# Performance work log

Hardware: AMD Instinct MI355X
Metric: run time of the kernel (lower is better)

Reference implementation:

```python
import jax, jax.numpy as jnp
import numpy as np

E, S, D, A, L, H, C = 8, 6000, 128, 16, 64, 256, 64
B = 50            # no_batches hardcoded in torch forward
T = S // B        # number of outer integration steps
DT = 0.5          # solver dt; t_horizon=[0,1] -> 2 reversible-Heun substeps
NSUB = 2
SQDT = float(np.sqrt(DT))


def setup_inputs():
    ks = jax.random.split(jax.random.key(0), 24)
    w = lambda k, shp, s=0.05: (jax.random.normal(k, shp) * s).astype(jnp.float32)
    z = lambda shp: jnp.zeros(shp, jnp.float32)
    return dict(
        xs=w(ks[0], (E, S, D), 1.0),
        actions=w(ks[1], (E, S, A), 1.0),
        z0_noise=w(ks[2], (T, E, B, L), 1.0),
        dW=w(ks[3], (T, NSUB, E * B, L), 1.0),
        enc_w1=w(ks[4], (E, D, H)), enc_b1=z((E, H)),
        enc_w2=w(ks[5], (E, H, C)), enc_b2=z((E, C)),
        qz0_w=w(ks[6], (E, C, 2 * L)), qz0_b=z((E, 2 * L)),
        act_w=w(ks[7], (E, L + A + D, L)), act_b=z((E, L)),
        fw1=w(ks[8], (L, H)), fb1=z((H,)),
        fw2=w(ks[9], (H, H)), fb2=z((H,)),
        fw3=w(ks[10], (H, L)), fb3=z((L,)),
        hw1=w(ks[11], (L, H)), hb1=z((H,)),
        hw2=w(ks[12], (H, H)), hb2=z((H,)),
        hw3=w(ks[13], (H, L)), hb3=z((L,)),
        gw1=w(ks[14], (L, H)), gb1=z((L, H)),
        gw2=w(ks[15], (L, H), 0.02), gb2=jnp.ones((L,), jnp.float32),
        pw1=w(ks[16], (E, L, H)), pb1=z((E, H)),
        pw2=w(ks[17], (E, H, H)), pb2=z((E, H)),
        pw3=w(ks[18], (E, H, D)), pb3=z((E, D)),
        pz0_mean=z((E, 1, L)), pz0_logstd=z((E, 1, L)),
    )


def reference(xs, actions, z0_noise, dW,
              enc_w1, enc_b1, enc_w2, enc_b2, qz0_w, qz0_b, act_w, act_b,
              fw1, fb1, fw2, fb2, fw3, fb3, hw1, hb1, hw2, hb2, hw3, hb3,
              gw1, gb1, gw2, gb2, pw1, pb1, pw2, pb2, pw3, pb3,
              pz0_mean, pz0_logstd):
    xs_r = xs.reshape(E, T, B, D).transpose(1, 0, 2, 3)       # [T,E,B,D]
    act_r = actions.reshape(E, T, B, A).transpose(1, 0, 2, 3)  # [T,E,B,A]

    def mlp3(y, w1, b1, w2, b2, w3, b3):
        h1 = jax.nn.sigmoid(y @ w1 + b1)
        h2 = jax.nn.sigmoid(h1 @ w2 + b2)
        return h2 @ w3 + b3

    def g_fn(y):  # per-latent-dim diagonal diffusion nets, vectorized over L
        hc = jax.nn.sigmoid(y[..., None] * gw1 + gb1)          # [N,L,H]
        return jnp.sum(hc * gw2, axis=-1) + gb2                # [N,L]

    def drift_all(zc):
        fz = mlp3(zc, fw1, fb1, fw2, fb2, fw3, fb3)
        hz = mlp3(zc, hw1, hb1, hw2, hb2, hw3, hb3)
        gz = g_fn(zc)
        u = (fz - hz) / gz
        return fz, gz, 0.5 * jnp.sum(u * u, axis=-1)           # logqp drift

    def sde_solve(zini, dWs):  # reversible Heun, Stratonovich, logqp-augmented
        zc = zh = zini
        lc = lh = jnp.zeros(zini.shape[0], zini.dtype)
        fz, gz, lf = drift_all(zc)
        for k in range(NSUB):
            dWk = dWs[k] * SQDT
            zh_n = 2.0 * zc - zh + fz * DT + gz * dWk
            lh_n = 2.0 * lc - lh + lf * DT
            fz1, gz1, lf1 = drift_all(zh_n)
            zc = zc + 0.5 * (fz + fz1) * DT + 0.5 * (gz + gz1) * dWk
            lc = lc + 0.5 * (lf + lf1) * DT
            zh, lh, fz, gz, lf = zh_n, lh_n, fz1, gz1, lf1
        return zc, lc

    def step(z_prev, inp):
        i, x_i, a_i, n_i, dW_i = inp
        c1 = jax.nn.sigmoid(jnp.einsum('ebd,edh->ebh', x_i, enc_w1) + enc_b1[:, None])
        ctx = jnp.einsum('ebh,ehc->ebc', c1, enc_w2) + enc_b2[:, None]
        q = jnp.einsum('ebc,eck->ebk', ctx, qz0_w) + qz0_b[:, None]
        qm, ql = q[..., :L], q[..., L:]
        z0 = qm + jnp.exp(ql) * n_i
        z_in = jnp.where(i == 0, z0, z_prev)
        lat = jnp.concatenate([z_in, a_i, x_i], axis=-1)
        z_enc = jnp.einsum('ebf,efl->ebl', lat, act_w) + act_b[:, None]
        zf, lr = sde_solve(z_enc.reshape(E * B, L), dW_i)
        z_new = zf.reshape(E, B, L)
        p1 = jax.nn.sigmoid(jnp.einsum('ebl,elh->ebh', z_new, pw1) + pb1[:, None])
        p2 = jax.nn.sigmoid(jnp.einsum('ebh,ehk->ebk', p1, pw2) + pb2[:, None])
        xm = jnp.einsum('ebh,ehd->ebd', p2, pw3) + pb3[:, None]
        # KL(q(z0) || p(z0)) elementwise, p has mean pz0_mean, logstd pz0_logstd
        kl = (pz0_logstd - ql
              + (jnp.exp(2.0 * ql) + (qm - pz0_mean) ** 2) / (2.0 * jnp.exp(2.0 * pz0_logstd))
              - 0.5)
        logqp0 = kl.sum(-1).mean(-1)  # [E]
        return z_new, (xm, lr.reshape(E, B), logqp0)

    z_init = jnp.zeros((E, B, L), xs.dtype)
    _, (xm_all, lr_all, lq0_all) = jax.lax.scan(
        step, z_init, (jnp.arange(T), xs_r, act_r, z0_noise, dW))
    predicted_xs = xm_all.transpose(1, 0, 2, 3).reshape(E, T * B, D)
    logqp_path = lr_all.mean(-1).sum(0) + lq0_all.sum(0)  # [E]
    return logqp_path, predicted_xs
```

## Files before the change

### kernel.cpp

```cpp
#include <hip/hip_runtime.h>
#include <math.h>

#define E 8
#define S 6000
#define D 128
#define A 16
#define L 64
#define H 256
#define C 64
#define B 50
#define T 120
#define NSUB 2
#define FLAT 208
#define RTOT 400
#define RPB 10
#define NBLK (RTOT / RPB)
#define BGRP 10
#define NBG 5

#define DT 0.5f
#define SQDT 0.70710678118654752440f

#define GNT 4096
#define GYMIN (-128.0f)
#define GDY 0.0625f
#define GINVDY 16.0f

typedef __attribute__((ext_vector_type(8))) short bf16x8;
typedef __attribute__((ext_vector_type(4))) float f32x4;

#define MFMA16(a, b, c) __builtin_amdgcn_mfma_f32_16x16x32_bf16(a, b, c, 0, 0, 0)

__device__ __forceinline__ float sigf(float x) { return 1.0f / (1.0f + __expf(-x)); }

__device__ __forceinline__ unsigned short f2bf(float x) {
    union { float f; unsigned u; } v; v.f = x;
    unsigned r = (v.u + 0x7FFFu + ((v.u >> 16) & 1u)) >> 16;
    return (unsigned short)r;
}

__global__ void gtab_kernel(const float* __restrict__ gw1, const float* __restrict__ gb1,
                            const float* __restrict__ gw2, const float* __restrict__ gb2,
                            float* __restrict__ tab) {
    int idx = blockIdx.x * blockDim.x + threadIdx.x;
    if (idx >= L * GNT) return;
    int l = idx / GNT, i = idx % GNT;
    float y = GYMIN + (float)i * GDY;
    const float* w1 = gw1 + l * H;
    const float* b1 = gb1 + l * H;
    const float* w2 = gw2 + l * H;
    float acc = gb2[l];
    #pragma unroll 4
    for (int h = 0; h < H; ++h) acc += w2[h] * sigf(y * w1[h] + b1[h]);
    tab[idx] = acc;
}

__global__ void packB_kernel(const float* __restrict__ src, unsigned short* __restrict__ dst,
                             int K, int N) {
    int idx = blockIdx.x * 256 + threadIdx.x;
    if (idx >= K * N) return;
    int j = idx & 7;
    int lane = (idx >> 3) & 63;
    int t2 = idx >> 9;
    int KC = K >> 5;
    int kc = t2 % KC, n = t2 / KC;
    int k = (kc << 5) + ((lane >> 4) << 3) + j;
    int c = (n << 4) + (lane & 15);
    dst[idx] = f2bf(src[k * N + c]);
}

__global__ void packAW_kernel(const float* __restrict__ aw, unsigned short* __restrict__ dst) {
    int idx = blockIdx.x * 256 + threadIdx.x;
    if (idx >= E * L * L) return;
    int e = idx >> 12;
    int rem = idx & 4095;
    int j = rem & 7;
    int lane = (rem >> 3) & 63;
    int t2 = rem >> 9;
    int kc = t2 & 1, n = t2 >> 1;
    int k = (kc << 5) + ((lane >> 4) << 3) + j;
    int c = (n << 4) + (lane & 15);
    dst[idx] = f2bf(aw[((size_t)e * FLAT + k) * L + c]);
}

__global__ __launch_bounds__(256) void enc_kernel(const float* __restrict__ xs, const float* __restrict__ z0n,
                           const float* __restrict__ ew1, const float* __restrict__ eb1,
                           const float* __restrict__ ew2, const float* __restrict__ eb2,
                           const float* __restrict__ qw,  const float* __restrict__ qb,
                           const float* __restrict__ pm,  const float* __restrict__ pl,
                           float* __restrict__ z0buf, float* __restrict__ logqp0p) {
    int bid = blockIdx.x;
    int bg = bid % NBG; int te = bid / NBG; int e = te % E; int t = te / E;
    int tid = threadIdx.x;
    __shared__ float xsh[BGRP][D];
    __shared__ float c1s[BGRP][H];
    __shared__ float part[4][C][BGRP];
    __shared__ float ctxs[BGRP][C];
    __shared__ float qs[BGRP][2 * L];

    for (int i = tid; i < BGRP * D; i += 256) {
        int j = i / D, d = i % D;
        xsh[j][d] = xs[((size_t)e * S + (size_t)t * B + bg * BGRP + j) * D + d];
    }
    __syncthreads();
    {
        float bias = eb1[e * H + tid];
        float acc[BGRP];
        #pragma unroll
        for (int j = 0; j < BGRP; ++j) acc[j] = bias;
        const float* w = ew1 + (size_t)e * D * H + tid;
        #pragma unroll 4
        for (int d = 0; d < D; ++d) {
            float wv = w[(size_t)d * H];
            #pragma unroll
            for (int j = 0; j < BGRP; ++j) acc[j] += xsh[j][d] * wv;
        }
        #pragma unroll
        for (int j = 0; j < BGRP; ++j) c1s[j][tid] = sigf(acc[j]);
    }
    __syncthreads();
    {
        int c = tid & 63, kq = tid >> 6;
        float acc[BGRP];
        #pragma unroll
        for (int j = 0; j < BGRP; ++j) acc[j] = 0.f;
        const float* w = ew2 + (size_t)e * H * C + c;
        #pragma unroll 4
        for (int h = kq * 64; h < kq * 64 + 64; ++h) {
            float wv = w[(size_t)h * C];
            #pragma unroll
            for (int j = 0; j < BGRP; ++j) acc[j] += c1s[j][h] * wv;
        }
        #pragma unroll
        for (int j = 0; j < BGRP; ++j) part[kq][c][j] = acc[j];
    }
    __syncthreads();
    if (tid < C) {
        float bias = eb2[e * C + tid];
        #pragma unroll
        for (int j = 0; j < BGRP; ++j)
            ctxs[j][tid] = part[0][tid][j] + part[1][tid][j] + part[2][tid][j] + part[3][tid][j] + bias;
    }
    __syncthreads();
    if (tid < 2 * L) {
        float bias = qb[e * 2 * L + tid];
        float acc[BGRP];
        #pragma unroll
        for (int j = 0; j < BGRP; ++j) acc[j] = bias;
        const float* w = qw + (size_t)e * C * 2 * L + tid;
        #pragma unroll 4
        for (int c = 0; c < C; ++c) {
            float wv = w[(size_t)c * 2 * L];
            #pragma unroll
            for (int j = 0; j < BGRP; ++j) acc[j] += ctxs[j][c] * wv;
        }
        #pragma unroll
        for (int j = 0; j < BGRP; ++j) qs[j][tid] = acc[j];
    }
    __syncthreads();
    if (tid < L) {
        int l = tid;
        float kacc = 0.f;
        float m = pm[e * L + l], ls = pl[e * L + l];
        float inv2e = 1.0f / (2.0f * __expf(2.0f * ls));
        #pragma unroll
        for (int j = 0; j < BGRP; ++j) {
            float qm = qs[j][l], ql = qs[j][L + l];
            if (t == 0) {
                int b = bg * BGRP + j;
                float n = z0n[((size_t)e * B + b) * L + l];
                z0buf[((size_t)e * B + b) * L + l] = qm + __expf(ql) * n;
            }
            float dq = qm - m;
            kacc += ls - ql + (__expf(2.f * ql) + dq * dq) * inv2e - 0.5f;
        }
        #pragma unroll
        for (int off = 32; off; off >>= 1) kacc += __shfl_xor(kacc, off);
        if (l == 0) logqp0p[bid] = kacc / (float)B;
    }
}

__global__ __launch_bounds__(64) void ax_kernel(const float* __restrict__ xs, const float* __restrict__ actions,
                          const float* __restrict__ aw, const float* __restrict__ ab,
                          float* __restrict__ ax) {
    int bid = blockIdx.x;
    int bg = bid % NBG; int te = bid / NBG; int e = te % E; int t = te / E;
    int tid = threadIdx.x;
    __shared__ float xrow[BGRP][D];
    __shared__ float arow[BGRP][A];
    for (int i = tid; i < BGRP * D; i += 64) {
        int j = i / D, d = i % D;
        xrow[j][d] = xs[((size_t)e * S + (size_t)t * B + bg * BGRP + j) * D + d];
    }
    for (int i = tid; i < BGRP * A; i += 64) {
        int j = i / A, a = i % A;
        arow[j][a] = actions[((size_t)e * S + (size_t)t * B + bg * BGRP + j) * A + a];
    }
    __syncthreads();
    int l = tid;
    float acc[BGRP];
    float bias = ab[e * L + l];
    #pragma unroll
    for (int j = 0; j < BGRP; ++j) acc[j] = bias;
    const float* awp = aw + ((size_t)e * FLAT + L) * L + l;
    #pragma unroll 4
    for (int a = 0; a < A; ++a) {
        float wv = awp[(size_t)a * L];
        #pragma unroll
        for (int j = 0; j < BGRP; ++j) acc[j] += arow[j][a] * wv;
    }
    const float* xwp = aw + ((size_t)e * FLAT + L + A) * L + l;
    #pragma unroll 4
    for (int d = 0; d < D; ++d) {
        float wv = xwp[(size_t)d * L];
        #pragma unroll
        for (int j = 0; j < BGRP; ++j) acc[j] += xrow[j][d] * wv;
    }
    size_t rbase = (size_t)t * RTOT + e * B + bg * BGRP;
    #pragma unroll
    for (int j = 0; j < BGRP; ++j) ax[(rbase + j) * L + l] = acc[j];
}

__global__ __launch_bounds__(1024, 4) void seq_kernel(
    const unsigned short* __restrict__ pkAW, const float* __restrict__ dW,
    const float* __restrict__ z0buf, const float* __restrict__ axbuf,
    const unsigned short* __restrict__ pk1, const unsigned short* __restrict__ pk2,
    const unsigned short* __restrict__ pk3,
    const float* __restrict__ fb1, const float* __restrict__ hb1,
    const float* __restrict__ fb2, const float* __restrict__ hb2,
    const float* __restrict__ fb3, const float* __restrict__ hb3,
    const float* __restrict__ gtab, float* __restrict__ z_all, float* __restrict__ rowlr)
{
    __shared__ __align__(16) bf16x8 w1L[64 * 64];
    __shared__ __align__(16) bf16x8 w0L[8 * 64];
    __shared__ __align__(16) unsigned short ybf[16 * 64];
    __shared__ __align__(16) unsigned short o1[2][16 * 256];
    __shared__ __align__(16) unsigned short o2[2][16 * 256];
    __shared__ float fh2[2][2][16][64];
    __shared__ float zcS[16][64];

    int tid = threadIdx.x;
    int wv = tid >> 6;
    int lane = tid & 63;
    int rA = lane & 15, kg = lane >> 4;
    int sw = (rA & 7) << 3;
    int r_base = blockIdx.x * RPB;
    int e = blockIdx.x / 5;

    int net = wv >> 3;
    int na = (wv & 7) << 1;
    int cnet = wv >> 3, crem = wv & 7, n0c = crem >> 1, khc = crem & 1;

    {
        const bf16x8* p1 = (const bf16x8*)pk1;
        #pragma unroll
        for (int f = 0; f < 4; ++f)
            w1L[(((wv << 2) + f) << 6) + lane] =
                p1[net * 2048 + ((na + (f >> 1)) * 2 + (f & 1)) * 64 + lane];
        if (wv < 4) {
            const bf16x8* p0 = (const bf16x8*)pkAW + (e << 9);
            w0L[(((wv << 1) + 0) << 6) + lane] = p0[(wv * 2 + 0) * 64 + lane];
            w0L[(((wv << 1) + 1) << 6) + lane] = p0[(wv * 2 + 1) * 64 + lane];
        }
    }
    bf16x8 W2r[16], W3r[4];
    {
        const bf16x8* p2 = (const bf16x8*)pk2 + net * 8192;
        #pragma unroll
        for (int i2 = 0; i2 < 2; ++i2)
            #pragma unroll
            for (int kc = 0; kc < 8; ++kc)
                W2r[i2 * 8 + kc] = p2[((na + i2) * 8 + kc) * 64 + lane];
        const bf16x8* p3 = (const bf16x8*)pk3 + cnet * 2048;
        #pragma unroll
        for (int kc = 0; kc < 4; ++kc)
            W3r[kc] = p3[(n0c * 8 + khc * 4 + kc) * 64 + lane];
    }
    float biasA0, biasA1, biasB0, biasB1, biasC;
    {
        const float* b1 = net ? hb1 : fb1;
        const float* b2 = net ? hb2 : fb2;
        const float* b3 = cnet ? hb3 : fb3;
        biasA0 = b1[((na + 0) << 4) + rA];
        biasA1 = b1[((na + 1) << 4) + rA];
        biasB0 = b2[((na + 0) << 4) + rA];
        biasB1 = b2[((na + 1) << 4) + rA];
        biasC = khc ? 0.f : b3[(n0c << 4) + rA];
    }

    int orow = tid >> 6, ol = tid & 63;
    bool owner = (tid < RPB * L);
    float zc_r = 0.f, zh_r = 0.f, fz_r = 0.f, gz_r = 1.f, lf_r = 0.f;
    float lcacc = 0.f, lrs = 0.f;
    float gt0 = 1.f, gt1 = 1.f, gfr = 0.f;
    float ax_r = 0.f, dwA_r = 0.f, dwB_r = 0.f;

    for (int i = tid; i < 16 * 64; i += 1024) {
        int r = i >> 6;
        float v = (i < RPB * L) ? z0buf[(size_t)r_base * L + i] : 0.f;
        ybf[i ^ ((r & 7) << 3)] = f2bf(v);
    }
    __syncthreads();

    auto gprep = [&](float v) {
        float x = (v - GYMIN) * GINVDY;
        x = fminf(fmaxf(x, 0.0f), (float)(GNT - 2) + 0.999f);
        int ii = (int)x;
        gfr = x - (float)ii;
        const float* tl = gtab + ((size_t)ol << 12);
        gt0 = tl[ii];
        gt1 = tl[ii + 1];
    };

    auto drift3 = [&]() {
        {
            bf16x8 A0 = *(const bf16x8*)&ybf[((rA << 6) + (kg << 3)) ^ sw];
            bf16x8 A1 = *(const bf16x8*)&ybf[((rA << 6) + 32 + (kg << 3)) ^ sw];
            f32x4 acc0 = (f32x4){biasA0, biasA0, biasA0, biasA0};
            f32x4 acc1 = (f32x4){biasA1, biasA1, biasA1, biasA1};
            acc0 = MFMA16(A0, w1L[(((wv << 2) + 0) << 6) + lane], acc0);
            acc0 = MFMA16(A1, w1L[(((wv << 2) + 1) << 6) + lane], acc0);
            acc1 = MFMA16(A0, w1L[(((wv << 2) + 2) << 6) + lane], acc1);
            acc1 = MFMA16(A1, w1L[(((wv << 2) + 3) << 6) + lane], acc1);
            unsigned short* o1n = o1[net];
            int c0 = ((na + 0) << 4) + rA;
            int c1 = ((na + 1) << 4) + rA;
            #pragma unroll
            for (int rr = 0; rr < 4; ++rr) {
                int r = (kg << 2) + rr;
                int rx = (r & 7) << 3;
                o1n[((r << 8) + c0) ^ rx] = f2bf(sigf(acc0[rr]));
                o1n[((r << 8) + c1) ^ rx] = f2bf(sigf(acc1[rr]));
            }
        }
        __syncthreads();
        {
            const unsigned short* o1n = o1[net];
            f32x4 acc0 = (f32x4){biasB0, biasB0, biasB0, biasB0};
            f32x4 acc1 = (f32x4){biasB1, biasB1, biasB1, biasB1};
            #pragma unroll
            for (int kc = 0; kc < 8; ++kc) {
                bf16x8 Ak = *(const bf16x8*)&o1n[((rA << 8) + (kc << 5) + (kg << 3)) ^ sw];
                acc0 = MFMA16(Ak, W2r[kc], acc0);
                acc1 = MFMA16(Ak, W2r[8 + kc], acc1);
            }
            unsigned short* o2n = o2[net];
            int c0 = ((na + 0) << 4) + rA;
            int c1 = ((na + 1) << 4) + rA;
            #pragma unroll
            for (int rr = 0; rr < 4; ++rr) {
                int r = (kg << 2) + rr;
                int rx = (r & 7) << 3;
                o2n[((r << 8) + c0) ^ rx] = f2bf(sigf(acc0[rr]));
                o2n[((r << 8) + c1) ^ rx] = f2bf(sigf(acc1[rr]));
            }
        }
        __syncthreads();
        {
            const unsigned short* o2n = o2[cnet];
            f32x4 acc = (f32x4){biasC, biasC, biasC, biasC};
            #pragma unroll
            for (int kc = 0; kc < 4; ++kc) {
                bf16x8 Ak = *(const bf16x8*)&o2n[((rA << 8) + (((khc << 2) + kc) << 5) + (kg << 3)) ^ sw];
                acc = MFMA16(Ak, W3r[kc], acc);
            }
            int c = (n0c << 4) + rA;
            #pragma unroll
            for (int rr = 0; rr < 4; ++rr)
                fh2[cnet][khc][(kg << 2) + rr][c] = acc[rr];
        }
        __syncthreads();
    };

    for (int t = 0; t < T; ++t) {
        if (owner) {
            ax_r  = axbuf[((size_t)t * RTOT + r_base) * L + tid];
            dwA_r = dW[((size_t)(t * 2 + 0) * RTOT + r_base) * L + tid] * SQDT;
            dwB_r = dW[((size_t)(t * 2 + 1) * RTOT + r_base) * L + tid] * SQDT;
        }
        if (wv < 4) {
            bf16x8 Z0 = *(const bf16x8*)&ybf[((rA << 6) + (kg << 3)) ^ sw];
            bf16x8 Z1 = *(const bf16x8*)&ybf[((rA << 6) + 32 + (kg << 3)) ^ sw];
            f32x4 acc = (f32x4){0.f, 0.f, 0.f, 0.f};
            acc = MFMA16(Z0, w0L[((wv << 1) << 6) + lane], acc);
            acc = MFMA16(Z1, w0L[(((wv << 1) + 1) << 6) + lane], acc);
            int c = (wv << 4) + rA;
            #pragma unroll
            for (int rr = 0; rr < 4; ++rr)
                zcS[(kg << 2) + rr][c] = acc[rr];
        }
        __syncthreads();
        if (owner) {
            float v = zcS[orow][ol] + ax_r;
            zc_r = v;
            ybf[tid ^ ((orow & 7) << 3)] = f2bf(v);
            gprep(v);
        }
        __syncthreads();

        #pragma unroll
        for (int d = 0; d < 3; ++d) {
            drift3();
            if (owner) {
                float fv = fh2[0][0][orow][ol] + fh2[0][1][orow][ol];
                float hv = fh2[1][0][orow][ol] + fh2[1][1][orow][ol];
                float gv = gt0 * (1.0f - gfr) + gt1 * gfr;
                float uu = (fv - hv) / gv;
                float us = uu * uu;
                #pragma unroll
                for (int off = 32; off; off >>= 1) us += __shfl_xor(us, off);
                float lfd = 0.5f * us;
                if (d == 0) {
                    fz_r = fv; gz_r = gv; lf_r = lfd;
                    float y1 = zc_r + fv * DT + gv * dwA_r;
                    zh_r = y1;
                    ybf[tid ^ ((orow & 7) << 3)] = f2bf(y1);
                    gprep(y1);
                } else if (d == 1) {
                    zc_r += 0.5f * (fz_r + fv) * DT + 0.5f * (gz_r + gv) * dwA_r;
                    lcacc = 0.5f * (lf_r + lfd) * DT;
                    float y2 = 2.f * zc_r - zh_r + fv * DT + gv * dwB_r;
                    fz_r = fv; gz_r = gv; lf_r = lfd;
                    ybf[tid ^ ((orow & 7) << 3)] = f2bf(y2);
                    gprep(y2);
                } else {
                    zc_r += 0.5f * (fz_r + fv) * DT + 0.5f * (gz_r + gv) * dwB_r;
                    lcacc += 0.5f * (lf_r + lfd) * DT;
                    lrs += lcacc;
                    z_all[((size_t)t * RTOT + r_base) * L + tid] = zc_r;
                    ybf[tid ^ ((orow & 7) << 3)] = f2bf(zc_r);
                }
            }
            __syncthreads();
        }
    }
    if (owner && ol == 0) rowlr[r_base + orow] = lrs;
}

__global__ __launch_bounds__(256) void proj_kernel(const float* __restrict__ z_all,
                            const float* __restrict__ pw1, const float* __restrict__ pb1,
                            const float* __restrict__ pw2, const float* __restrict__ pb2,
                            const float* __restrict__ pw3, const float* __restrict__ pb3,
                            float* __restrict__ out) {
    int bid = blockIdx.x;
    int bg = bid % NBG; int te = bid / NBG; int e = te % E; int t = te / E;
    int tid = threadIdx.x;
    __shared__ float zs[BGRP][L];
    __shared__ float p1s[BGRP][H];
    __shared__ float p2s[BGRP][H];
    __shared__ float part3[D][BGRP];
    size_t rbase = (size_t)t * RTOT + e * B + bg * BGRP;
    for (int i = tid; i < BGRP * L; i += 256) {
        int j = i >> 6, ll = i & 63;
        zs[j][ll] = z_all[(rbase + j) * L + ll];
    }
    __syncthreads();
    {
        float bias = pb1[e * H + tid];
        float acc[BGRP];
        #pragma unroll
        for (int j = 0; j < BGRP; ++j) acc[j] = bias;
        const float* w = pw1 + (size_t)e * L * H + tid;
        #pragma unroll 4
        for (int k = 0; k < L; ++k) {
            float wv = w[(size_t)k * H];
            #pragma unroll
            for (int j = 0; j < BGRP; ++j) acc[j] += zs[j][k] * wv;
        }
        #pragma unroll
        for (int j = 0; j < BGRP; ++j) p1s[j][tid] = sigf(acc[j]);
    }
    __syncthreads();
    {
        float bias = pb2[e * H + tid];
        float acc[BGRP];
        #pragma unroll
        for (int j = 0; j < BGRP; ++j) acc[j] = bias;
        const float* w = pw2 + (size_t)e * H * H + tid;
        #pragma unroll 4
        for (int k = 0; k < H; ++k) {
            float wv = w[(size_t)k * H];
            #pragma unroll
            for (int j = 0; j < BGRP; ++j) acc[j] += p1s[j][k] * wv;
        }
        #pragma unroll
        for (int j = 0; j < BGRP; ++j) p2s[j][tid] = sigf(acc[j]);
    }
    __syncthreads();
    float acc3[BGRP];
    {
        int dd = tid & 127, kh = tid >> 7;
        #pragma unroll
        for (int j = 0; j < BGRP; ++j) acc3[j] = 0.f;
        const float* w = pw3 + (size_t)e * H * D + dd;
        #pragma unroll 4
        for (int k = kh * 128; k < kh * 128 + 128; ++k) {
            float wv = w[(size_t)k * D];
            #pragma unroll
            for (int j = 0; j < BGRP; ++j) acc3[j] += p2s[j][k] * wv;
        }
        if (kh == 1) {
            #pragma unroll
            for (int j = 0; j < BGRP; ++j) part3[dd][j] = acc3[j];
        }
    }
    __syncthreads();
    if (tid < D) {
        float bias = pb3[e * D + tid];
        #pragma unroll
        for (int j = 0; j < BGRP; ++j) {
            out[8 + ((size_t)e * S + (size_t)t * B + bg * BGRP + j) * D + tid]
                = acc3[j] + part3[tid][j] + bias;
        }
    }
}

__global__ void fin_kernel(const float* __restrict__ logqp0p, const float* __restrict__ rowlr,
                           float* __restrict__ out) {
    int e = threadIdx.x;
    if (e < E) {
        float acc = 0.f;
        for (int t = 0; t < T; ++t)
            for (int bg = 0; bg < NBG; ++bg)
                acc += logqp0p[(t * E + e) * NBG + bg];
        float s = 0.f;
        for (int b = 0; b < B; ++b) s += rowlr[e * B + b];
        out[e] = acc + s / (float)B;
    }
}

extern "C" void kernel_launch(void* const* d_in, const int* in_sizes, int n_in,
                              void* d_out, int out_size, void* d_ws, size_t ws_size,
                              hipStream_t stream) {
    const float* xs      = (const float*)d_in[0];
    const float* actions = (const float*)d_in[1];
    const float* z0n     = (const float*)d_in[2];
    const float* dWp     = (const float*)d_in[3];
    const float* ew1     = (const float*)d_in[4];
    const float* eb1     = (const float*)d_in[5];
    const float* ew2     = (const float*)d_in[6];
    const float* eb2     = (const float*)d_in[7];
    const float* qw      = (const float*)d_in[8];
    const float* qb      = (const float*)d_in[9];
    const float* aw      = (const float*)d_in[10];
    const float* ab      = (const float*)d_in[11];
    const float* fw1     = (const float*)d_in[12];
    const float* fb1     = (const float*)d_in[13];
    const float* fw2     = (const float*)d_in[14];
    const float* fb2     = (const float*)d_in[15];
    const float* fw3     = (const float*)d_in[16];
    const float* fb3     = (const float*)d_in[17];
    const float* hw1     = (const float*)d_in[18];
    const float* hb1     = (const float*)d_in[19];
    const float* hw2     = (const float*)d_in[20];
    const float* hb2     = (const float*)d_in[21];
    const float* hw3     = (const float*)d_in[22];
    const float* hb3     = (const float*)d_in[23];
    const float* gw1     = (const float*)d_in[24];
    const float* gb1     = (const float*)d_in[25];
    const float* gw2     = (const float*)d_in[26];
    const float* gb2     = (const float*)d_in[27];
    const float* pw1     = (const float*)d_in[28];
    const float* pb1     = (const float*)d_in[29];
    const float* pw2     = (const float*)d_in[30];
    const float* pb2     = (const float*)d_in[31];
    const float* pw3     = (const float*)d_in[32];
    const float* pb3     = (const float*)d_in[33];
    const float* pm      = (const float*)d_in[34];
    const float* pl      = (const float*)d_in[35];

    float* ws      = (float*)d_ws;
    float* z0buf   = ws;
    float* axbuf   = z0buf + 25600;
    float* z_all   = axbuf + 3072000;
    float* logqp0p = z_all + 3072000;
    float* rowlr   = logqp0p + 4800;
    float* gtab    = rowlr + 400;
    unsigned short* pku = (unsigned short*)(gtab + 262144);
    unsigned short* pk1 = pku;
    unsigned short* pk2 = pk1 + 32768;
    unsigned short* pk3 = pk2 + 131072;
    unsigned short* pkAW = pk3 + 32768;
    float* out     = (float*)d_out;

    packB_kernel<<<64,  256, 0, stream>>>(fw1, pk1,          64, 256);
    packB_kernel<<<64,  256, 0, stream>>>(hw1, pk1 + 16384,  64, 256);
    packB_kernel<<<256, 256, 0, stream>>>(fw2, pk2,          256, 256);
    packB_kernel<<<256, 256, 0, stream>>>(hw2, pk2 + 65536,  256, 256);
    packB_kernel<<<64,  256, 0, stream>>>(fw3, pk3,          256, 64);
    packB_kernel<<<64,  256, 0, stream>>>(hw3, pk3 + 16384,  256, 64);
    packAW_kernel<<<128, 256, 0, stream>>>(aw, pkAW);
    gtab_kernel<<<1024, 256, 0, stream>>>(gw1, gb1, gw2, gb2, gtab);
    enc_kernel<<<T * E * NBG, 256, 0, stream>>>(xs, z0n, ew1, eb1, ew2, eb2, qw, qb, pm, pl, z0buf, logqp0p);
    ax_kernel<<<T * E * NBG, 64, 0, stream>>>(xs, actions, aw, ab, axbuf);
    seq_kernel<<<NBLK, 1024, 0, stream>>>(pkAW, dWp, z0buf, axbuf,
                                          pk1, pk2, pk3,
                                          fb1, hb1, fb2, hb2, fb3, hb3,
                                          gtab, z_all, rowlr);
    proj_kernel<<<T * E * NBG, 256, 0, stream>>>(z_all, pw1, pb1, pw2, pb2, pw3, pb3, out);
    fin_kernel<<<1, 64, 0, stream>>>(logqp0p, rowlr, out);
}
```

Before: 2.973 ms.

## Trim barriers and defer logqp reduction in the sequential SDE kernel

Restructures the serial SDE loop in several ways. The z-encoder MFMA now writes directly into the drift input with the ax term added in-register, which removes one block barrier per step. A second ybf buffer separates the carried state from the drift input. The per-substep logqp wavefront shuffle-reduction is replaced by a per-lane weighted accumulation that is reduced once at the end. __syncthreads is replaced by a custom barrier that waits only on LDS counters, and the encoder weights are held in registers. The risks are ordering hazards with the lighter barrier and a change in floating-point summation order.

```diff
diff --git a/kernel.cpp b/kernel.cpp
--- a/kernel.cpp
+++ b/kernel.cpp
@@ -39,6 +39,12 @@
     return (unsigned short)r;
 }
 
+__device__ __forceinline__ void bar_lgkm() {
+    asm volatile("s_waitcnt lgkmcnt(0)" ::: "memory");
+    __builtin_amdgcn_s_barrier();
+    __builtin_amdgcn_sched_barrier(0);
+}
+
 __global__ void gtab_kernel(const float* __restrict__ gw1, const float* __restrict__ gb1,
                             const float* __restrict__ gw2, const float* __restrict__ gb2,
                             float* __restrict__ tab) {
@@ -231,11 +237,11 @@
     const float* __restrict__ fb3, const float* __restrict__ hb3,
     const float* __restrict__ gtab, float* __restrict__ z_all, float* __restrict__ rowlr)
 {
-    __shared__ __align__(16) bf16x8 w1L[64 * 64];
-    __shared__ __align__(16) bf16x8 w0L[8 * 64];
-    __shared__ __align__(16) unsigned short ybf[16 * 64];
-    __shared__ __align__(16) unsigned short o1[2][16 * 256];
-    __shared__ __align__(16) unsigned short o2[2][16 * 256];
+    __shared__ __align__(16) bf16x8 w1L[4096];
+    __shared__ __align__(16) unsigned short ybfA[1024];
+    __shared__ __align__(16) unsigned short ybfZ[1024];
+    __shared__ __align__(16) unsigned short o1[2][4096];
+    __shared__ __align__(16) unsigned short o2[2][4096];
     __shared__ float fh2[2][2][16][64];
     __shared__ float zcS[16][64];
 
@@ -247,23 +253,20 @@
     int r_base = blockIdx.x * RPB;
     int e = blockIdx.x / 5;
 
+    for (int i = tid; i < 4096; i += 1024) w1L[i] = ((const bf16x8*)pk1)[i];
+
     int net = wv >> 3;
     int na = (wv & 7) << 1;
     int cnet = wv >> 3, crem = wv & 7, n0c = crem >> 1, khc = crem & 1;
-
-    {
-        const bf16x8* p1 = (const bf16x8*)pk1;
-        #pragma unroll
-        for (int f = 0; f < 4; ++f)
-            w1L[(((wv << 2) + f) << 6) + lane] =
-                p1[net * 2048 + ((na + (f >> 1)) * 2 + (f & 1)) * 64 + lane];
-        if (wv < 4) {
-            const bf16x8* p0 = (const bf16x8*)pkAW + (e << 9);
-            w0L[(((wv << 1) + 0) << 6) + lane] = p0[(wv * 2 + 0) * 64 + lane];
-            w0L[(((wv << 1) + 1) << 6) + lane] = p0[(wv * 2 + 1) * 64 + lane];
-        }
-    }
-    bf16x8 W2r[16], W3r[4];
+    int nZ = wv & 3;
+    int lZ = (nZ << 4) + rA;
+
+    bf16x8 W0r0 = {}, W0r1 = {}, W2r[16], W3r[4];
+    if (wv < 4) {
+        const bf16x8* p0 = (const bf16x8*)pkAW + (e << 9);
+        W0r0 = p0[(nZ * 2 + 0) * 64 + lane];
+        W0r1 = p0[(nZ * 2 + 1) * 64 + lane];
+    }
     {
         const bf16x8* p2 = (const bf16x8*)pk2 + net * 8192;
         #pragma unroll
@@ -290,15 +293,15 @@
 
     int orow = tid >> 6, ol = tid & 63;
     bool owner = (tid < RPB * L);
-    float zc_r = 0.f, zh_r = 0.f, fz_r = 0.f, gz_r = 1.f, lf_r = 0.f;
-    float lcacc = 0.f, lrs = 0.f;
+    float zc_r = 0.f, zh_r = 0.f, fz_r = 0.f, gz_r = 1.f;
+    float dwA_r = 0.f, dwB_r = 0.f;
     float gt0 = 1.f, gt1 = 1.f, gfr = 0.f;
-    float ax_r = 0.f, dwA_r = 0.f, dwB_r = 0.f;
-
-    for (int i = tid; i < 16 * 64; i += 1024) {
-        int r = i >> 6;
-        float v = (i < RPB * L) ? z0buf[(size_t)r_base * L + i] : 0.f;
-        ybf[i ^ ((r & 7) << 3)] = f2bf(v);
+    float scal = 0.f;
+
+    {
+        int r = tid >> 6;
+        float v = (tid < RPB * L) ? z0buf[(size_t)r_base * L + tid] : 0.f;
+        ybfZ[tid ^ ((r & 7) << 3)] = f2bf(v);
     }
     __syncthreads();
 
@@ -312,129 +315,131 @@
         gt1 = tl[ii + 1];
     };
 
-    auto drift3 = [&]() {
-        {
-            bf16x8 A0 = *(const bf16x8*)&ybf[((rA << 6) + (kg << 3)) ^ sw];
-            bf16x8 A1 = *(const bf16x8*)&ybf[((rA << 6) + 32 + (kg << 3)) ^ sw];
-            f32x4 acc0 = (f32x4){biasA0, biasA0, biasA0, biasA0};
-            f32x4 acc1 = (f32x4){biasA1, biasA1, biasA1, biasA1};
-            acc0 = MFMA16(A0, w1L[(((wv << 2) + 0) << 6) + lane], acc0);
-            acc0 = MFMA16(A1, w1L[(((wv << 2) + 1) << 6) + lane], acc0);
-            acc1 = MFMA16(A0, w1L[(((wv << 2) + 2) << 6) + lane], acc1);
-            acc1 = MFMA16(A1, w1L[(((wv << 2) + 3) << 6) + lane], acc1);
-            unsigned short* o1n = o1[net];
-            int c0 = ((na + 0) << 4) + rA;
-            int c1 = ((na + 1) << 4) + rA;
+    for (int t = 0; t < T; ++t) {
+        if (wv < 4) {
+            float axv[4];
             #pragma unroll
             for (int rr = 0; rr < 4; ++rr) {
                 int r = (kg << 2) + rr;
-                int rx = (r & 7) << 3;
-                o1n[((r << 8) + c0) ^ rx] = f2bf(sigf(acc0[rr]));
-                o1n[((r << 8) + c1) ^ rx] = f2bf(sigf(acc1[rr]));
-            }
-        }
-        __syncthreads();
-        {
-            const unsigned short* o1n = o1[net];
-            f32x4 acc0 = (f32x4){biasB0, biasB0, biasB0, biasB0};
-            f32x4 acc1 = (f32x4){biasB1, biasB1, biasB1, biasB1};
-            #pragma unroll
-            for (int kc = 0; kc < 8; ++kc) {
-                bf16x8 Ak = *(const bf16x8*)&o1n[((rA << 8) + (kc << 5) + (kg << 3)) ^ sw];
-                acc0 = MFMA16(Ak, W2r[kc], acc0);
-                acc1 = MFMA16(Ak, W2r[8 + kc], acc1);
-            }
-            unsigned short* o2n = o2[net];
-            int c0 = ((na + 0) << 4) + rA;
-            int c1 = ((na + 1) << 4) + rA;
+                axv[rr] = (r < RPB) ? axbuf[((size_t)t * RTOT + r_base + r) * L + lZ] : 0.f;
+            }
+            bf16x8 Z0 = *(const bf16x8*)&ybfZ[((rA << 6) + (kg << 3)) ^ sw];
+            bf16x8 Z1 = *(const bf16x8*)&ybfZ[((rA << 6) + 32 + (kg << 3)) ^ sw];
+            f32x4 acc = (f32x4){0.f, 0.f, 0.f, 0.f};
+            acc = MFMA16(Z0, W0r0, acc);
+            acc = MFMA16(Z1, W0r1, acc);
             #pragma unroll
             for (int rr = 0; rr < 4; ++rr) {
                 int r = (kg << 2) + rr;
-                int rx = (r & 7) << 3;
-                o2n[((r << 8) + c0) ^ rx] = f2bf(sigf(acc0[rr]));
-                o2n[((r << 8) + c1) ^ rx] = f2bf(sigf(acc1[rr]));
-            }
-        }
-        __syncthreads();
-        {
-            const unsigned short* o2n = o2[cnet];
-            f32x4 acc = (f32x4){biasC, biasC, biasC, biasC};
-            #pragma unroll
-            for (int kc = 0; kc < 4; ++kc) {
-                bf16x8 Ak = *(const bf16x8*)&o2n[((rA << 8) + (((khc << 2) + kc) << 5) + (kg << 3)) ^ sw];
-                acc = MFMA16(Ak, W3r[kc], acc);
-            }
-            int c = (n0c << 4) + rA;
-            #pragma unroll
-            for (int rr = 0; rr < 4; ++rr)
-                fh2[cnet][khc][(kg << 2) + rr][c] = acc[rr];
-        }
-        __syncthreads();
-    };
-
-    for (int t = 0; t < T; ++t) {
-        if (owner) {
-            ax_r  = axbuf[((size_t)t * RTOT + r_base) * L + tid];
-            dwA_r = dW[((size_t)(t * 2 + 0) * RTOT + r_base) * L + tid] * SQDT;
-            dwB_r = dW[((size_t)(t * 2 + 1) * RTOT + r_base) * L + tid] * SQDT;
-        }
-        if (wv < 4) {
-            bf16x8 Z0 = *(const bf16x8*)&ybf[((rA << 6) + (kg << 3)) ^ sw];
-            bf16x8 Z1 = *(const bf16x8*)&ybf[((rA << 6) + 32 + (kg << 3)) ^ sw];
-            f32x4 acc = (f32x4){0.f, 0.f, 0.f, 0.f};
-            acc = MFMA16(Z0, w0L[((wv << 1) << 6) + lane], acc);
-            acc = MFMA16(Z1, w0L[(((wv << 1) + 1) << 6) + lane], acc);
-            int c = (wv << 4) + rA;
-            #pragma unroll
-            for (int rr = 0; rr < 4; ++rr)
-                zcS[(kg << 2) + rr][c] = acc[rr];
-        }
-        __syncthreads();
-        if (owner) {
-            float v = zcS[orow][ol] + ax_r;
-            zc_r = v;
-            ybf[tid ^ ((orow & 7) << 3)] = f2bf(v);
-            gprep(v);
-        }
-        __syncthreads();
+                float v = acc[rr] + axv[rr];
+                zcS[r][lZ] = v;
+                ybfA[((r << 6) + lZ) ^ ((r & 7) << 3)] = f2bf(v);
+            }
+        }
+        bar_lgkm();
 
         #pragma unroll
         for (int d = 0; d < 3; ++d) {
-            drift3();
+            if (d == 0 && owner) {
+                zc_r = zcS[orow][ol];
+                zh_r = zc_r;
+                gprep(zc_r);
+                dwA_r = dW[((size_t)(2 * t) * RTOT + r_base + orow) * L + ol] * SQDT;
+                dwB_r = dW[((size_t)(2 * t + 1) * RTOT + r_base + orow) * L + ol] * SQDT;
+            }
+            {
+                bf16x8 A0 = *(const bf16x8*)&ybfA[((rA << 6) + (kg << 3)) ^ sw];
+                bf16x8 A1 = *(const bf16x8*)&ybfA[((rA << 6) + 32 + (kg << 3)) ^ sw];
+                f32x4 acc0 = (f32x4){biasA0, biasA0, biasA0, biasA0};
+                f32x4 acc1 = (f32x4){biasA1, biasA1, biasA1, biasA1};
+                acc0 = MFMA16(A0, w1L[net * 2048 + ((na + 0) * 2 + 0) * 64 + lane], acc0);
+                acc0 = MFMA16(A1, w1L[net * 2048 + ((na + 0) * 2 + 1) * 64 + lane], acc0);
+                acc1 = MFMA16(A0, w1L[net * 2048 + ((na + 1) * 2 + 0) * 64 + lane], acc1);
+                acc1 = MFMA16(A1, w1L[net * 2048 + ((na + 1) * 2 + 1) * 64 + lane], acc1);
+                unsigned short* o1n = o1[net];
+                int c0 = ((na + 0) << 4) + rA;
+                int c1 = ((na + 1) << 4) + rA;
+                #pragma unroll
+                for (int rr = 0; rr < 4; ++rr) {
+                    int r = (kg << 2) + rr;
+                    int rx = (r & 7) << 3;
+                    o1n[((r << 8) + c0) ^ rx] = f2bf(sigf(acc0[rr]));
+                    o1n[((r << 8) + c1) ^ rx] = f2bf(sigf(acc1[rr]));
+                }
+            }
+            bar_lgkm();
+            {
+                const unsigned short* o1n = o1[net];
+                f32x4 acc0 = (f32x4){biasB0, biasB0, biasB0, biasB0};
+                f32x4 acc1 = (f32x4){biasB1, biasB1, biasB1, biasB1};
+                #pragma unroll
+                for (int kc = 0; kc < 8; ++kc) {
+                    bf16x8 Ak = *(const bf16x8*)&o1n[((rA << 8) + (kc << 5) + (kg << 3)) ^ sw];
+                    acc0 = MFMA16(Ak, W2r[kc], acc0);
+                    acc1 = MFMA16(Ak, W2r[8 + kc], acc1);
+                }
+                unsigned short* o2n = o2[net];
+                int c0 = ((na + 0) << 4) + rA;
+                int c1 = ((na + 1) << 4) + rA;
+                #pragma unroll
+                for (int rr = 0; rr < 4; ++rr) {
+                    int r = (kg << 2) + rr;
+                    int rx = (r & 7) << 3;
+                    o2n[((r << 8) + c0) ^ rx] = f2bf(sigf(acc0[rr]));
+                    o2n[((r << 8) + c1) ^ rx] = f2bf(sigf(acc1[rr]));
+                }
+            }
+            bar_lgkm();
+            {
+                const unsigned short* o2n = o2[cnet];
+                f32x4 acc = (f32x4){biasC, biasC, biasC, biasC};
+                #pragma unroll
+                for (int kc = 0; kc < 4; ++kc) {
+                    bf16x8 Ak = *(const bf16x8*)&o2n[((rA << 8) + (((khc << 2) + kc) << 5) + (kg << 3)) ^ sw];
+                    acc = MFMA16(Ak, W3r[kc], acc);
+                }
+                int c = (n0c << 4) + rA;
+                #pragma unroll
+                for (int rr = 0; rr < 4; ++rr)
+                    fh2[cnet][khc][(kg << 2) + rr][c] = acc[rr];
+            }
+            bar_lgkm();
             if (owner) {
                 float fv = fh2[0][0][orow][ol] + fh2[0][1][orow][ol];
                 float hv = fh2[1][0][orow][ol] + fh2[1][1][orow][ol];
                 float gv = gt0 * (1.0f - gfr) + gt1 * gfr;
                 float uu = (fv - hv) / gv;
                 float us = uu * uu;
-                #pragma unroll
-                for (int off = 32; off; off >>= 1) us += __shfl_xor(us, off);
-                float lfd = 0.5f * us;
                 if (d == 0) {
-                    fz_r = fv; gz_r = gv; lf_r = lfd;
+                    scal += us;
+                    fz_r = fv; gz_r = gv;
                     float y1 = zc_r + fv * DT + gv * dwA_r;
                     zh_r = y1;
-                    ybf[tid ^ ((orow & 7) << 3)] = f2bf(y1);
+                    ybfA[tid ^ ((orow & 7) << 3)] = f2bf(y1);
                     gprep(y1);
                 } else if (d == 1) {
                     zc_r += 0.5f * (fz_r + fv) * DT + 0.5f * (gz_r + gv) * dwA_r;
-                    lcacc = 0.5f * (lf_r + lfd) * DT;
+                    scal += 2.0f * us;
                     float y2 = 2.f * zc_r - zh_r + fv * DT + gv * dwB_r;
-                    fz_r = fv; gz_r = gv; lf_r = lfd;
-                    ybf[tid ^ ((orow & 7) << 3)] = f2bf(y2);
+                    fz_r = fv; gz_r = gv;
+                    ybfA[tid ^ ((orow & 7) << 3)] = f2bf(y2);
                     gprep(y2);
                 } else {
                     zc_r += 0.5f * (fz_r + fv) * DT + 0.5f * (gz_r + gv) * dwB_r;
-                    lcacc += 0.5f * (lf_r + lfd) * DT;
-                    lrs += lcacc;
+                    scal += us;
                     z_all[((size_t)t * RTOT + r_base) * L + tid] = zc_r;
-                    ybf[tid ^ ((orow & 7) << 3)] = f2bf(zc_r);
+                    ybfZ[tid ^ ((orow & 7) << 3)] = f2bf(zc_r);
                 }
             }
-            __syncthreads();
-        }
-    }
-    if (owner && ol == 0) rowlr[r_base + orow] = lrs;
+            bar_lgkm();
+        }
+    }
+    if (owner) {
+        float s = scal;
+        #pragma unroll
+        for (int off = 32; off; off >>= 1) s += __shfl_xor(s, off);
+        if (ol == 0) rowlr[r_base + orow] = 0.25f * DT * s;
+    }
 }
 
 __global__ __launch_bounds__(256) void proj_kernel(const float* __restrict__ z_all,
```

Result: slower. 3.107 ms (+4.5%).
